# Kernel optimization log

Hardware: AMD Instinct MI355X
Metric: run time of the kernel (lower is better)

Reference implementation:

```python
import jax, jax.numpy as jnp
import numpy as np

# dims: batch B, seq T, model C, expert hidden H, num experts E, top-k K
B, T, C, H, E, K = 4, 1024, 1024, 1024, 8, 2


def _swiglu(x):
    a, b = jnp.split(x, 2, axis=-1)
    return jax.nn.silu(a) * b


def setup_inputs() -> dict:
    key = jax.random.key(0)
    ks = jax.random.split(key, 6)
    s = 0.02
    x = jax.random.normal(ks[0], (B, T, C), jnp.float32)
    # weights stored [in, out] (transpose of torch Linear layout; same math y = x @ W)
    w_shared_in = jax.random.normal(ks[1], (C, 2 * H), jnp.float32) * s
    w_shared_out = jax.random.normal(ks[2], (H, C), jnp.float32) * s
    w1_shared = jax.random.normal(ks[3], (C, 2 * H), jnp.float32) * s
    w2 = jax.random.normal(ks[4], (E, H, C), jnp.float32) * s  # stacked routed_w2
    w_gate = jax.random.normal(ks[5], (C, E), jnp.float32) * s
    gate_bias = jnp.zeros((E,), jnp.float32)  # buffer, updated only in training
    return {
        "x": x,
        "w_shared_in": w_shared_in,
        "w_shared_out": w_shared_out,
        "w1_shared": w1_shared,
        "w2": w2,
        "w_gate": w_gate,
        "gate_bias": gate_bias,
    }


def reference(x, w_shared_in, w_shared_out, w1_shared, w2, w_gate, gate_bias):
    Bx, Tx, Cx = x.shape
    S = Bx * Tx
    fx = x.reshape(S, Cx)  # [S, C]

    # shared expert: SwiGLU MLP
    shared_out = _swiglu(fx @ w_shared_in) @ w_shared_out  # [S, C]

    # router: softmax(top-k) over biased logits
    logits = fx @ w_gate + gate_bias  # [S, E]
    probs = jax.nn.softmax(logits, axis=-1)
    top_val, top_idx = jax.lax.top_k(probs, K)  # [S, K]

    # dense dispatch-weight matrix [S, E] (zero where expert not selected)
    wdense = jnp.zeros((S, E), probs.dtype).at[
        jnp.arange(S)[:, None], top_idx
    ].add(top_val)

    # routed experts share w1_shared, so the SwiGLU hidden is identical for all
    # experts; compute it once for every token, then apply per-expert w2.
    hid = _swiglu(fx @ w1_shared)  # [S, H]
    routed_out = jnp.zeros_like(shared_out)
    for e in range(E):  # small fixed expert count
        routed_out = routed_out + wdense[:, e:e + 1] * (hid @ w2[e])

    return (shared_out + routed_out).reshape(Bx, Tx, Cx)
```

## Files before the change

### kernel.cpp

```cpp
#include <hip/hip_runtime.h>
#include <stdint.h>

typedef __attribute__((ext_vector_type(4))) float f32x4;
typedef __attribute__((ext_vector_type(8))) short s16x8;

static constexpr int S_TOK = 4096;
static constexpr int CDIM  = 1024;
static constexpr int HDIM  = 1024;
static constexpr int H2    = 2048;
static constexpr int NEXP  = 8;

#define MAXRT2 40

__device__ __forceinline__ unsigned short f2bf(float f) {
  union { float f; uint32_t u; } c; c.f = f;
  uint32_t u = c.u;
  u += 0x7fffu + ((u >> 16) & 1u);
  return (unsigned short)(u >> 16);
}

__device__ __forceinline__ float bf2f(unsigned short u) {
  return __uint_as_float(((uint32_t)u) << 16);
}

__device__ __forceinline__ void gload16(const void* g, void* l) {
  __builtin_amdgcn_global_load_lds(
      (const __attribute__((address_space(1))) void*)g,
      (__attribute__((address_space(3))) void*)l, 16, 0, 0);
}

__global__ __launch_bounds__(256) void prep_kernel(
    const float* __restrict__ x, const float* __restrict__ wsi,
    const float* __restrict__ w1s, const float* __restrict__ wso,
    const float* __restrict__ w2,
    unsigned short* __restrict__ xb, unsigned short* __restrict__ w12i,
    unsigned short* __restrict__ wso_t, unsigned short* __restrict__ w2t) {
  __shared__ float t[32][33];
  const int b = blockIdx.x;
  const int tid = threadIdx.x;

  if (b < 512) {
    const int n4 = S_TOK * CDIM / 4;
    for (int i = b * 256 + tid; i < n4; i += 512 * 256) {
      float4 v = reinterpret_cast<const float4*>(x)[i];
      ushort4 o;
      o.x = f2bf(v.x); o.y = f2bf(v.y); o.z = f2bf(v.z); o.w = f2bf(v.w);
      reinterpret_cast<ushort4*>(xb)[i] = o;
    }
    return;
  }
  if (b < 4608) {
    const int b2 = b - 512;
    const float* src = (b2 >= 2048) ? w1s : wsi;
    const int halfoff = (b2 >= 2048) ? 2048 : 0;
    const int rem = b2 & 2047;
    const int r0 = (rem >> 6) * 32;
    const int c0 = (rem & 63) * 32;
#pragma unroll
    for (int i = 0; i < 4; ++i) {
      int idx = tid + i * 256;
      int r = idx >> 5, c = idx & 31;
      t[r][c] = src[(size_t)(r0 + r) * H2 + c0 + c];
    }
    __syncthreads();
#pragma unroll
    for (int i = 0; i < 4; ++i) {
      int idx = tid + i * 256;
      int r = idx >> 5, c = idx & 31;
      const int ccol = c0 + r;
      const int part = ccol >> 10, h = ccol & 1023;
      const int drow = halfoff + (h & 15) + ((h >> 4) << 5) + (part << 4);
      w12i[(size_t)drow * CDIM + r0 + c] = f2bf(t[c][r]);
    }
    return;
  }
  const float* src;
  unsigned short* dst;
  int bx, by;
  if (b < 5632) {
    const int b3 = b - 4608;
    src = wso; dst = wso_t; by = b3 >> 5; bx = b3 & 31;
  } else {
    const int b4 = b - 5632;
    const int z = b4 >> 10;
    const int rem = b4 & 1023;
    src = w2 + (size_t)z * HDIM * CDIM;
    dst = w2t + (size_t)z * HDIM * CDIM;
    by = rem >> 5; bx = rem & 31;
  }
  const int r0 = by * 32, c0 = bx * 32;
#pragma unroll
  for (int i = 0; i < 4; ++i) {
    int idx = tid + i * 256;
    int r = idx >> 5, c = idx & 31;
    t[r][c] = src[(size_t)(r0 + r) * CDIM + c0 + c];
  }
  __syncthreads();
#pragma unroll
  for (int i = 0; i < 4; ++i) {
    int idx = tid + i * 256;
    int r = idx >> 5, c = idx & 31;
    dst[(size_t)(c0 + r) * HDIM + r0 + c] = f2bf(t[c][r]);
  }
}

__global__ void router_kernel(const float* __restrict__ x, const float* __restrict__ wg,
                              const float* __restrict__ gb,
                              int2* __restrict__ ti_e, float2* __restrict__ ti_w) {
  const int l = threadIdx.x & 63;
  const int wid = threadIdx.x >> 6;
  const int s = blockIdx.x * 4 + wid;
  const float* xr = x + (size_t)s * CDIM;
  float acc[NEXP];
#pragma unroll
  for (int e = 0; e < NEXP; ++e) acc[e] = 0.f;
  for (int c = l; c < CDIM; c += 64) {
    float xv = xr[c];
    const float* wr_ = wg + (size_t)c * NEXP;
#pragma unroll
    for (int e = 0; e < NEXP; ++e) acc[e] += xv * wr_[e];
  }
#pragma unroll
  for (int e = 0; e < NEXP; ++e) {
#pragma unroll
    for (int off = 32; off > 0; off >>= 1) acc[e] += __shfl_xor(acc[e], off);
    acc[e] += gb[e];
  }
  float m = acc[0];
#pragma unroll
  for (int e = 1; e < NEXP; ++e) m = fmaxf(m, acc[e]);
  float ex[NEXP], sum = 0.f;
#pragma unroll
  for (int e = 0; e < NEXP; ++e) { ex[e] = __expf(acc[e] - m); sum += ex[e]; }
  int i0 = 0;
#pragma unroll
  for (int e = 1; e < NEXP; ++e) if (acc[e] > acc[i0]) i0 = e;
  int i1 = (i0 == 0) ? 1 : 0;
#pragma unroll
  for (int e = 0; e < NEXP; ++e) {
    if (e == i0) continue;
    if (acc[e] > acc[i1]) i1 = e;
  }
  if (l == 0) {
    const float inv = 1.f / sum;
    ti_e[s] = make_int2(i0, i1);
    ti_w[s] = make_float2(ex[i0] * inv, ex[i1] * inv);
  }
}

__global__ __launch_bounds__(1024) void build_kernel(
    const int2* __restrict__ ti_e,
    int* __restrict__ cnt, int* __restrict__ offs,
    int* __restrict__ gidx, int2* __restrict__ ti_slot) {
  __shared__ int gcnt[64][NEXP];
  __shared__ int gbase[64][NEXP];
  __shared__ int eoff[NEXP];
  const int tid = threadIdx.x;
  const int wid = tid >> 6, lane = tid & 63;

  for (int p = 0; p < 4; ++p) {
    const int g = p * 16 + wid;
    const int2 e = ti_e[g * 64 + lane];
#pragma unroll
    for (int ex = 0; ex < NEXP; ++ex) {
      uint64_t b0 = __ballot(e.x == ex);
      uint64_t b1 = __ballot(e.y == ex);
      if (lane == 0) gcnt[g][ex] = __popcll(b0) + __popcll(b1);
    }
  }
  __syncthreads();
  if (tid < NEXP) {
    const int ex = tid;
    int a = 0;
    for (int g = 0; g < 64; ++g) { gbase[g][ex] = a; a += gcnt[g][ex]; }
    eoff[ex] = a;
  }
  __syncthreads();
  if (tid == 0) {
    int a = 0;
#pragma unroll
    for (int ex = 0; ex < NEXP; ++ex) {
      const int c = eoff[ex];
      offs[ex] = a; cnt[ex] = c; eoff[ex] = a; a += c;
    }
    offs[NEXP] = a;
  }
  __syncthreads();
  for (int p = 0; p < 4; ++p) {
    const int g = p * 16 + wid;
    const int s = g * 64 + lane;
    const int2 e = ti_e[s];
    const uint64_t below = (lane == 0) ? 0ull : (~0ull >> (64 - lane));
    const uint64_t beloweq = below | (1ull << lane);
    int slot0 = 0, slot1 = 0;
#pragma unroll
    for (int ex = 0; ex < NEXP; ++ex) {
      uint64_t b0 = __ballot(e.x == ex);
      uint64_t b1 = __ballot(e.y == ex);
      const int base = gbase[g][ex];
      if (e.x == ex) slot0 = base + __popcll(b0 & below) + __popcll(b1 & below);
      if (e.y == ex) slot1 = base + __popcll(b0 & beloweq) + __popcll(b1 & below);
    }
    ti_slot[s] = make_int2(slot0, slot1);
    gidx[eoff[e.x] + slot0] = s;
    gidx[eoff[e.y] + slot1] = s;
  }
}

template<bool LAST>
__device__ __forceinline__ void iter8(
    const unsigned short* a00, const unsigned short* a01,
    const unsigned short* a10, const unsigned short* a11,
    const unsigned short* b00, const unsigned short* b01,
    const unsigned short* b10, const unsigned short* b11,
    unsigned short* SA, unsigned short* SB,
    int e, int t8, int awb, int bwb, int ak0, int ak1,
    f32x4 (&acc)[8][4]) {
  const int o = e + 1;
  s16x8 a[4][2], bl[2][2], bh[2][2];

#define LD_A4(d, F0) { _Pragma("unroll") for (int f_ = 0; f_ < 4; ++f_) { \
    const unsigned short* p_ = SA + (d) * 16384 + awb + ((F0) + f_) * 1024; \
    a[f_][0] = *reinterpret_cast<const s16x8*>(p_ + ak0); \
    a[f_][1] = *reinterpret_cast<const s16x8*>(p_ + ak1); } }
#define LD_B2(d, bb, N0) { _Pragma("unroll") for (int n_ = 0; n_ < 2; ++n_) { \
    const unsigned short* p_ = SB + (d) * 16384 + bwb + ((N0) + n_) * 1024; \
    bb[n_][0] = *reinterpret_cast<const s16x8*>(p_ + ak0); \
    bb[n_][1] = *reinterpret_cast<const s16x8*>(p_ + ak1); } }
#define STG2(S, d, h, p0, p1, kt) { \
    gload16((p0) + (size_t)(kt) * 64, (S) + (d) * 16384 + (h) * 8192 + t8); \
    gload16((p1) + (size_t)(kt) * 64, (S) + (d) * 16384 + (h) * 8192 + 4096 + t8); }
#define QUAD(F0, bb, N0) { _Pragma("unroll") for (int k_ = 0; k_ < 2; ++k_) \
    { _Pragma("unroll") for (int f_ = 0; f_ < 4; ++f_) \
      { _Pragma("unroll") for (int n_ = 0; n_ < 2; ++n_) \
        acc[(F0) + f_][(N0) + n_] = __builtin_amdgcn_mfma_f32_16x16x32_bf16( \
            a[f_][k_], bb[n_][k_], acc[(F0) + f_][(N0) + n_], 0, 0, 0); } } }
#define PH_MID() { asm volatile("" ::: "memory"); __builtin_amdgcn_s_barrier(); \
    asm volatile("s_waitcnt lgkmcnt(0)" ::: "memory"); __builtin_amdgcn_s_setprio(1); }
#define PH_END() { __builtin_amdgcn_s_setprio(0); asm volatile("" ::: "memory"); \
    __builtin_amdgcn_s_barrier(); asm volatile("" ::: "memory"); }

  LD_A4(0, 0) LD_B2(0, bl, 0)
  STG2(SA, 1, 0, a00, a01, o) STG2(SA, 1, 1, a10, a11, o)
  PH_MID() QUAD(0, bl, 0) PH_END()
  LD_B2(0, bh, 2)
  PH_MID() QUAD(0, bh, 2) PH_END()
  LD_A4(0, 4)
  if (!LAST) STG2(SB, 0, 0, b00, b01, e + 2)
  PH_MID() QUAD(4, bh, 2) PH_END()
  if (!LAST) {
    STG2(SB, 0, 1, b10, b11, e + 2)
    asm volatile("s_waitcnt vmcnt(4)" ::: "memory");
  } else {
    asm volatile("s_waitcnt vmcnt(0)" ::: "memory");
  }
  PH_MID() QUAD(4, bl, 0) PH_END()
  LD_A4(1, 0) LD_B2(1, bl, 0)
  if (!LAST) STG2(SA, 0, 0, a00, a01, e + 2)
  PH_MID() QUAD(0, bl, 0) PH_END()
  LD_B2(1, bh, 2)
  if (!LAST) STG2(SA, 0, 1, a10, a11, e + 2)
  PH_MID() QUAD(0, bh, 2) PH_END()
  LD_A4(1, 4)
  if (!LAST) STG2(SB, 1, 0, b00, b01, o + 2)
  PH_MID() QUAD(4, bh, 2) PH_END()
  if (!LAST) {
    STG2(SB, 1, 1, b10, b11, o + 2)
    asm volatile("s_waitcnt vmcnt(4)" ::: "memory");
  }
  PH_MID() QUAD(4, bl, 0) PH_END()

#undef LD_A4
#undef LD_B2
#undef STG2
#undef QUAD
#undef PH_MID
#undef PH_END
}

__device__ __forceinline__ void prologue8(
    const unsigned short* a00, const unsigned short* a01,
    const unsigned short* a10, const unsigned short* a11,
    const unsigned short* b00, const unsigned short* b01,
    const unsigned short* b10, const unsigned short* b11,
    unsigned short* SA, unsigned short* SB, int t8) {
  gload16(a00, SA + t8);                gload16(a01, SA + 4096 + t8);
  gload16(a10, SA + 8192 + t8);         gload16(a11, SA + 8192 + 4096 + t8);
  gload16(b00, SB + t8);                gload16(b01, SB + 4096 + t8);
  gload16(b10, SB + 8192 + t8);         gload16(b11, SB + 8192 + 4096 + t8);
  gload16(b00 + 64, SB + 16384 + t8);   gload16(b01 + 64, SB + 16384 + 4096 + t8);
  gload16(b10 + 64, SB + 16384 + 8192 + t8);
  gload16(b11 + 64, SB + 16384 + 8192 + 4096 + t8);
  asm volatile("s_waitcnt vmcnt(4)" ::: "memory");
  asm volatile("" ::: "memory");
  __builtin_amdgcn_s_barrier();
  asm volatile("" ::: "memory");
}

__global__ __launch_bounds__(512, 2) void gemm1_kernel(
    const unsigned short* __restrict__ xb, const unsigned short* __restrict__ w12i,
    unsigned short* __restrict__ Hs, unsigned short* __restrict__ Hr) {
  __shared__ unsigned short SA[32768];
  __shared__ unsigned short SB[32768];
  const int tid = threadIdx.x;
  const int l = tid & 63, wid = tid >> 6;
  const int wm = wid >> 2, wn = wid & 3;
  const int lr = l & 15;
  const int awb = wm * 8192 + lr * 64;
  const int bwb = wn * 4096 + lr * 64;
  const int ak0 = (((l >> 4) << 3)) ^ ((l & 7) << 3);
  const int ak1 = 32 ^ ak0;
  const int hw = blockIdx.y * gridDim.x + blockIdx.x;
  const int logical = (hw & 7) * 32 + (hw >> 3);
  const int m0 = (logical >> 4) * 256;
  const int n0 = (logical & 15) * 256;
  const int srow = tid >> 3;
  const int scol = (((tid & 7) ^ (srow & 7)) << 3);
  const int t8 = tid * 8;
  f32x4 acc[8][4] = {};
  const unsigned short* a00 = xb + (size_t)(m0 + srow) * CDIM + scol;
  const unsigned short* a01 = a00 + (size_t)64 * CDIM;
  const unsigned short* a10 = a00 + (size_t)128 * CDIM;
  const unsigned short* a11 = a00 + (size_t)192 * CDIM;
  const unsigned short* b00 = w12i + (size_t)(n0 + srow) * CDIM + scol;
  const unsigned short* b01 = b00 + (size_t)64 * CDIM;
  const unsigned short* b10 = b00 + (size_t)128 * CDIM;
  const unsigned short* b11 = b00 + (size_t)192 * CDIM;

  prologue8(a00, a01, a10, a11, b00, b01, b10, b11, SA, SB, t8);
  for (int it = 0; it < 7; ++it)
    iter8<false>(a00, a01, a10, a11, b00, b01, b10, b11, SA, SB, 2 * it,
                 t8, awb, bwb, ak0, ak1, acc);
  iter8<true>(a00, a01, a10, a11, b00, b01, b10, b11, SA, SB, 14,
              t8, awb, bwb, ak0, ak1, acc);

  unsigned short* Hbuf = (n0 < 2048) ? Hs : Hr;
  const int rb = m0 + wm * 128 + ((l >> 4) << 2);
  const int hbase = ((n0 & 2047) >> 1) + wn * 32;
#pragma unroll
  for (int fm = 0; fm < 8; ++fm)
#pragma unroll
    for (int j = 0; j < 2; ++j)
#pragma unroll
      for (int r = 0; r < 4; ++r) {
        float av = acc[fm][2 * j][r];
        float bv = acc[fm][2 * j + 1][r];
        float hv = (av / (1.f + __expf(-av))) * bv;
        Hbuf[(size_t)(rb + fm * 16 + r) * HDIM + hbase + j * 16 + lr] = f2bf(hv);
      }
}

__global__ __launch_bounds__(512, 2) void gemm2_kernel(
    const unsigned short* __restrict__ Hs, const unsigned short* __restrict__ Hr,
    const unsigned short* __restrict__ wso_t, const unsigned short* __restrict__ w2t,
    const int* __restrict__ cnt, const int* __restrict__ offs, const int* __restrict__ gidx,
    unsigned short* __restrict__ Dout, unsigned short* __restrict__ Eout) {
  __shared__ unsigned short SA[32768];
  __shared__ unsigned short SB[32768];
  const int tid = threadIdx.x;
  const int l = tid & 63, wid = tid >> 6;
  const int wm = wid >> 2, wn = wid & 3;
  const int lr = l & 15;
  const int awb = wm * 8192 + lr * 64;
  const int bwb = wn * 4096 + lr * 64;
  const int ak0 = (((l >> 4) << 3)) ^ ((l & 7) << 3);
  const int ak1 = 32 ^ ak0;
  const int hw = blockIdx.y * gridDim.x + blockIdx.x;
  const int logical = (hw & 7) * 28 + (hw >> 3);
  const int gx = logical >> 2;
  const int n0 = (logical & 3) * 256;
  const int srow = tid >> 3;
  const int scol = (((tid & 7) ^ (srow & 7)) << 3);
  const int t8 = tid * 8;
  f32x4 acc[8][4] = {};

  const unsigned short *a00, *a01, *a10, *a11, *b00, *b01, *b10, *b11;
  int e = 0, cnte = 0, mt = 0, base = 0;
  const bool dense = (gx < 16);
  if (dense) {
    const int m0 = gx * 256;
    a00 = Hs + (size_t)(m0 + srow) * HDIM + scol;
    a01 = a00 + (size_t)64 * HDIM;
    a10 = a00 + (size_t)128 * HDIM;
    a11 = a00 + (size_t)192 * HDIM;
    b00 = wso_t + (size_t)(n0 + srow) * HDIM + scol;
    b01 = b00 + (size_t)64 * HDIM;
    b10 = b00 + (size_t)128 * HDIM;
    b11 = b00 + (size_t)192 * HDIM;
  } else {
    int t = gx - 16;
    bool found = false;
#pragma unroll
    for (int ee = 0; ee < NEXP; ++ee) {
      int c = cnt[ee];
      int nt = (c + 255) >> 8;
      if (!found) {
        if (t < nt) { e = ee; cnte = c; found = true; }
        else t -= nt;
      }
    }
    if (!found) return;
    mt = t;
    base = offs[e];
    const int r0 = mt * 256 + srow;
    const int t0 = gidx[base + min(r0,       cnte - 1)];
    const int t1 = gidx[base + min(r0 + 64,  cnte - 1)];
    const int t2 = gidx[base + min(r0 + 128, cnte - 1)];
    const int t3 = gidx[base + min(r0 + 192, cnte - 1)];
    a00 = Hr + (size_t)t0 * HDIM + scol;
    a01 = Hr + (size_t)t1 * HDIM + scol;
    a10 = Hr + (size_t)t2 * HDIM + scol;
    a11 = Hr + (size_t)t3 * HDIM + scol;
    b00 = w2t + (size_t)e * CDIM * HDIM + (size_t)(n0 + srow) * HDIM + scol;
    b01 = b00 + (size_t)64 * HDIM;
    b10 = b00 + (size_t)128 * HDIM;
    b11 = b00 + (size_t)192 * HDIM;
  }

  prologue8(a00, a01, a10, a11, b00, b01, b10, b11, SA, SB, t8);
  for (int it = 0; it < 7; ++it)
    iter8<false>(a00, a01, a10, a11, b00, b01, b10, b11, SA, SB, 2 * it,
                 t8, awb, bwb, ak0, ak1, acc);
  iter8<true>(a00, a01, a10, a11, b00, b01, b10, b11, SA, SB, 14,
              t8, awb, bwb, ak0, ak1, acc);

  const int rloc0 = wm * 128 + ((l >> 4) << 2);
  const int cb = n0 + wn * 64 + lr;
  if (dense) {
    const int rb = gx * 256 + rloc0;
#pragma unroll
    for (int fm = 0; fm < 8; ++fm)
#pragma unroll
      for (int fn = 0; fn < 4; ++fn)
#pragma unroll
        for (int r = 0; r < 4; ++r)
          Dout[(size_t)(rb + fm * 16 + r) * CDIM + cb + fn * 16] = f2bf(acc[fm][fn][r]);
  } else {
#pragma unroll
    for (int fm = 0; fm < 8; ++fm)
#pragma unroll
      for (int fn = 0; fn < 4; ++fn)
#pragma unroll
        for (int r = 0; r < 4; ++r) {
          const int rloc = mt * 256 + rloc0 + fm * 16 + r;
          if (rloc < cnte)
            Eout[(size_t)(base + rloc) * CDIM + cb + fn * 16] = f2bf(acc[fm][fn][r]);
        }
  }
}

__global__ void scatter_kernel(float* __restrict__ out, const unsigned short* __restrict__ Dout,
                               const unsigned short* __restrict__ Eout,
                               const int2* __restrict__ ti_e, const int2* __restrict__ ti_slot,
                               const float2* __restrict__ ti_w, const int* __restrict__ offs) {
  const int total = S_TOK * (CDIM / 8);
  int i = blockIdx.x * blockDim.x + threadIdx.x;
  const int st = gridDim.x * blockDim.x;
  for (; i < total; i += st) {
    const int s = i >> 7;
    const int j = (i & 127) << 3;
    const int2 e = ti_e[s];
    const int2 sl = ti_slot[s];
    const float2 wv = ti_w[s];
    const int p0 = offs[e.x] + sl.x;
    const int p1 = offs[e.y] + sl.y;
    const ushort4* d0 = reinterpret_cast<const ushort4*>(Dout + (size_t)s * CDIM + j);
    const ushort4* e0 = reinterpret_cast<const ushort4*>(Eout + (size_t)p0 * CDIM + j);
    const ushort4* e1 = reinterpret_cast<const ushort4*>(Eout + (size_t)p1 * CDIM + j);
    float* op = out + (size_t)s * CDIM + j;
#pragma unroll
    for (int q = 0; q < 2; ++q) {
      ushort4 dd = d0[q], a = e0[q], b = e1[q];
      float4 o;
      o.x = bf2f(dd.x) + wv.x * bf2f(a.x) + wv.y * bf2f(b.x);
      o.y = bf2f(dd.y) + wv.x * bf2f(a.y) + wv.y * bf2f(b.y);
      o.z = bf2f(dd.z) + wv.x * bf2f(a.z) + wv.y * bf2f(b.z);
      o.w = bf2f(dd.w) + wv.x * bf2f(a.w) + wv.y * bf2f(b.w);
      reinterpret_cast<float4*>(op)[q] = o;
    }
  }
}

extern "C" void kernel_launch(void* const* d_in, const int* in_sizes, int n_in,
                              void* d_out, int out_size, void* d_ws, size_t ws_size,
                              hipStream_t stream) {
  (void)in_sizes; (void)n_in; (void)out_size; (void)ws_size;
  const float* x   = (const float*)d_in[0];
  const float* wsi = (const float*)d_in[1];
  const float* wso = (const float*)d_in[2];
  const float* w1s = (const float*)d_in[3];
  const float* w2  = (const float*)d_in[4];
  const float* wg  = (const float*)d_in[5];
  const float* gb  = (const float*)d_in[6];
  float* out = (float*)d_out;

  char* w = (char*)d_ws;
  auto alloc = [&](size_t bytes) {
    char* p = w; w += (bytes + 255) & ~(size_t)255; return p;
  };
  unsigned short* xb    = (unsigned short*)alloc((size_t)S_TOK * CDIM * 2);
  unsigned short* w12i  = (unsigned short*)alloc((size_t)2 * H2 * CDIM * 2);
  unsigned short* wso_t = (unsigned short*)alloc((size_t)CDIM * HDIM * 2);
  unsigned short* w2t   = (unsigned short*)alloc((size_t)NEXP * CDIM * HDIM * 2);
  unsigned short* Hs    = (unsigned short*)alloc((size_t)S_TOK * HDIM * 2);
  unsigned short* Hr    = (unsigned short*)alloc((size_t)S_TOK * HDIM * 2);
  unsigned short* Dout  = (unsigned short*)alloc((size_t)S_TOK * CDIM * 2);
  unsigned short* Eout  = (unsigned short*)alloc((size_t)2 * S_TOK * CDIM * 2);
  int2*   ti_e   = (int2*)alloc((size_t)S_TOK * 8);
  int2*   ti_slot= (int2*)alloc((size_t)S_TOK * 8);
  float2* ti_w   = (float2*)alloc((size_t)S_TOK * 8);
  int*    cnt    = (int*)alloc(64);
  int*    offs   = (int*)alloc(64);
  int*    gidx   = (int*)alloc((size_t)2 * S_TOK * 4);

  router_kernel<<<S_TOK / 4, 256, 0, stream>>>(x, wg, gb, ti_e, ti_w);
  build_kernel<<<1, 1024, 0, stream>>>(ti_e, cnt, offs, gidx, ti_slot);

  prep_kernel<<<13824, 256, 0, stream>>>(x, wsi, w1s, wso, w2,
                                         xb, w12i, wso_t, w2t);

  gemm1_kernel<<<dim3(16, 16), 512, 0, stream>>>(xb, w12i, Hs, Hr);

  gemm2_kernel<<<dim3(16 + MAXRT2, CDIM / 256), 512, 0, stream>>>(
      Hs, Hr, wso_t, w2t, cnt, offs, gidx, Dout, Eout);

  scatter_kernel<<<2048, 256, 0, stream>>>(out, Dout, Eout, ti_e, ti_slot, ti_w, offs);
}
```

Baseline: 116.9 us.

## Fuse x bf16 conversion into router; 4-stage K-pipeline in gemm2

The router kernel now writes the bf16 copy of x while it reads x for the gate logits, so prep_kernel no longer makes a second pass over x. gemm2 is rewritten around a 4-slot ring of 32-wide K-chunks in shared memory with three loads in flight, explicit vmcnt waits, and direct global-to-LDS loads spread between MFMA groups under raised wave priority. The launch-bounds occupancy hint is dropped and the LDS swizzle changes. This is meant to hide memory latency better in the main expert GEMM, at the cost of one barrier per 32-K step and more hand-tuned scheduling that is easy to get wrong.

Measured after the change: 114.9 us. About the same (-1.8%).

```diff
diff --git a/kernel.cpp b/kernel.cpp
--- a/kernel.cpp
+++ b/kernel.cpp
@@ -30,30 +30,18 @@
 }
 
 __global__ __launch_bounds__(256) void prep_kernel(
-    const float* __restrict__ x, const float* __restrict__ wsi,
-    const float* __restrict__ w1s, const float* __restrict__ wso,
-    const float* __restrict__ w2,
-    unsigned short* __restrict__ xb, unsigned short* __restrict__ w12i,
-    unsigned short* __restrict__ wso_t, unsigned short* __restrict__ w2t) {
+    const float* __restrict__ wsi, const float* __restrict__ w1s,
+    const float* __restrict__ wso, const float* __restrict__ w2,
+    unsigned short* __restrict__ w12i, unsigned short* __restrict__ wso_t,
+    unsigned short* __restrict__ w2t) {
   __shared__ float t[32][33];
   const int b = blockIdx.x;
   const int tid = threadIdx.x;
 
-  if (b < 512) {
-    const int n4 = S_TOK * CDIM / 4;
-    for (int i = b * 256 + tid; i < n4; i += 512 * 256) {
-      float4 v = reinterpret_cast<const float4*>(x)[i];
-      ushort4 o;
-      o.x = f2bf(v.x); o.y = f2bf(v.y); o.z = f2bf(v.z); o.w = f2bf(v.w);
-      reinterpret_cast<ushort4*>(xb)[i] = o;
-    }
-    return;
-  }
-  if (b < 4608) {
-    const int b2 = b - 512;
-    const float* src = (b2 >= 2048) ? w1s : wsi;
-    const int halfoff = (b2 >= 2048) ? 2048 : 0;
-    const int rem = b2 & 2047;
+  if (b < 4096) {
+    const float* src = (b >= 2048) ? w1s : wsi;
+    const int halfoff = (b >= 2048) ? 2048 : 0;
+    const int rem = b & 2047;
     const int r0 = (rem >> 6) * 32;
     const int c0 = (rem & 63) * 32;
 #pragma unroll
@@ -77,11 +65,11 @@
   const float* src;
   unsigned short* dst;
   int bx, by;
-  if (b < 5632) {
-    const int b3 = b - 4608;
+  if (b < 5120) {
+    const int b3 = b - 4096;
     src = wso; dst = wso_t; by = b3 >> 5; bx = b3 & 31;
   } else {
-    const int b4 = b - 5632;
+    const int b4 = b - 5120;
     const int z = b4 >> 10;
     const int rem = b4 & 1023;
     src = w2 + (size_t)z * HDIM * CDIM;
@@ -106,16 +94,19 @@
 
 __global__ void router_kernel(const float* __restrict__ x, const float* __restrict__ wg,
                               const float* __restrict__ gb,
-                              int2* __restrict__ ti_e, float2* __restrict__ ti_w) {
+                              int2* __restrict__ ti_e, float2* __restrict__ ti_w,
+                              unsigned short* __restrict__ xb) {
   const int l = threadIdx.x & 63;
   const int wid = threadIdx.x >> 6;
   const int s = blockIdx.x * 4 + wid;
   const float* xr = x + (size_t)s * CDIM;
+  unsigned short* xbr = xb + (size_t)s * CDIM;
   float acc[NEXP];
 #pragma unroll
   for (int e = 0; e < NEXP; ++e) acc[e] = 0.f;
   for (int c = l; c < CDIM; c += 64) {
     float xv = xr[c];
+    xbr[c] = f2bf(xv);
     const float* wr_ = wg + (size_t)c * NEXP;
 #pragma unroll
     for (int e = 0; e < NEXP; ++e) acc[e] += xv * wr_[e];
@@ -350,43 +341,38 @@
       }
 }
 
-__global__ __launch_bounds__(512, 2) void gemm2_kernel(
+__global__ __launch_bounds__(512) void gemm2_kernel(
     const unsigned short* __restrict__ Hs, const unsigned short* __restrict__ Hr,
     const unsigned short* __restrict__ wso_t, const unsigned short* __restrict__ w2t,
     const int* __restrict__ cnt, const int* __restrict__ offs, const int* __restrict__ gidx,
     unsigned short* __restrict__ Dout, unsigned short* __restrict__ Eout) {
-  __shared__ unsigned short SA[32768];
-  __shared__ unsigned short SB[32768];
+  __shared__ unsigned short SA[4][2][4096];
+  __shared__ unsigned short SB[4][2][4096];
   const int tid = threadIdx.x;
   const int l = tid & 63, wid = tid >> 6;
   const int wm = wid >> 2, wn = wid & 3;
   const int lr = l & 15;
-  const int awb = wm * 8192 + lr * 64;
-  const int bwb = wn * 4096 + lr * 64;
-  const int ak0 = (((l >> 4) << 3)) ^ ((l & 7) << 3);
-  const int ak1 = 32 ^ ak0;
+  const int hi8 = (l >> 4) << 3;
+  const int wnh = wn >> 1;
+  const int wno = (wn & 1) << 6;
   const int hw = blockIdx.y * gridDim.x + blockIdx.x;
   const int logical = (hw & 7) * 28 + (hw >> 3);
   const int gx = logical >> 2;
   const int n0 = (logical & 3) * 256;
-  const int srow = tid >> 3;
-  const int scol = (((tid & 7) ^ (srow & 7)) << 3);
-  const int t8 = tid * 8;
   f32x4 acc[8][4] = {};
 
-  const unsigned short *a00, *a01, *a10, *a11, *b00, *b01, *b10, *b11;
+  const int srow = tid >> 2;
+  const int cs = (((tid & 3) ^ ((tid >> 3) & 3)) << 3);
+
+  const unsigned short *pa0, *pa1, *pb0, *pb1;
   int e = 0, cnte = 0, mt = 0, base = 0;
   const bool dense = (gx < 16);
   if (dense) {
     const int m0 = gx * 256;
-    a00 = Hs + (size_t)(m0 + srow) * HDIM + scol;
-    a01 = a00 + (size_t)64 * HDIM;
-    a10 = a00 + (size_t)128 * HDIM;
-    a11 = a00 + (size_t)192 * HDIM;
-    b00 = wso_t + (size_t)(n0 + srow) * HDIM + scol;
-    b01 = b00 + (size_t)64 * HDIM;
-    b10 = b00 + (size_t)128 * HDIM;
-    b11 = b00 + (size_t)192 * HDIM;
+    pa0 = Hs + (size_t)(m0 + srow) * HDIM + cs;
+    pa1 = pa0 + (size_t)128 * HDIM;
+    pb0 = wso_t + (size_t)(n0 + srow) * HDIM + cs;
+    pb1 = pb0 + (size_t)128 * HDIM;
   } else {
     int t = gx - 16;
     bool found = false;
@@ -403,26 +389,80 @@
     mt = t;
     base = offs[e];
     const int r0 = mt * 256 + srow;
-    const int t0 = gidx[base + min(r0,       cnte - 1)];
-    const int t1 = gidx[base + min(r0 + 64,  cnte - 1)];
-    const int t2 = gidx[base + min(r0 + 128, cnte - 1)];
-    const int t3 = gidx[base + min(r0 + 192, cnte - 1)];
-    a00 = Hr + (size_t)t0 * HDIM + scol;
-    a01 = Hr + (size_t)t1 * HDIM + scol;
-    a10 = Hr + (size_t)t2 * HDIM + scol;
-    a11 = Hr + (size_t)t3 * HDIM + scol;
-    b00 = w2t + (size_t)e * CDIM * HDIM + (size_t)(n0 + srow) * HDIM + scol;
-    b01 = b00 + (size_t)64 * HDIM;
-    b10 = b00 + (size_t)128 * HDIM;
-    b11 = b00 + (size_t)192 * HDIM;
-  }
-
-  prologue8(a00, a01, a10, a11, b00, b01, b10, b11, SA, SB, t8);
-  for (int it = 0; it < 7; ++it)
-    iter8<false>(a00, a01, a10, a11, b00, b01, b10, b11, SA, SB, 2 * it,
-                 t8, awb, bwb, ak0, ak1, acc);
-  iter8<true>(a00, a01, a10, a11, b00, b01, b10, b11, SA, SB, 14,
-              t8, awb, bwb, ak0, ak1, acc);
+    const int tok0 = gidx[base + min(r0, cnte - 1)];
+    const int tok1 = gidx[base + min(r0 + 128, cnte - 1)];
+    pa0 = Hr + (size_t)tok0 * HDIM + cs;
+    pa1 = Hr + (size_t)tok1 * HDIM + cs;
+    pb0 = w2t + (size_t)e * CDIM * HDIM + (size_t)(n0 + srow) * HDIM + cs;
+    pb1 = pb0 + (size_t)128 * HDIM;
+  }
+
+  const int t8 = tid * 8;
+#pragma unroll
+  for (int s = 0; s < 3; ++s) {
+    const int kk = s * 32;
+    gload16(pa0 + kk, &SA[s][0][t8]);
+    gload16(pa1 + kk, &SA[s][1][t8]);
+    gload16(pb0 + kk, &SB[s][0][t8]);
+    gload16(pb1 + kk, &SB[s][1][t8]);
+  }
+
+  for (int s = 0; s < 32; ++s) {
+    if (s < 30)       asm volatile("s_waitcnt vmcnt(8)" ::: "memory");
+    else if (s == 30) asm volatile("s_waitcnt vmcnt(4)" ::: "memory");
+    else              asm volatile("s_waitcnt vmcnt(0)" ::: "memory");
+    __builtin_amdgcn_s_barrier();
+    asm volatile("" ::: "memory");
+    const int c = s & 3;
+    const unsigned short* A_ = &SA[c][wm][0];
+    const unsigned short* B_ = &SB[c][wnh][0];
+    s16x8 a[8], b[4];
+#pragma unroll
+    for (int f = 0; f < 8; ++f) {
+      const int r = f * 16 + lr;
+      a[f] = *reinterpret_cast<const s16x8*>(&A_[r * 32 + (hi8 ^ (((r >> 1) & 3) << 3))]);
+    }
+#pragma unroll
+    for (int j = 0; j < 4; ++j) {
+      const int r = wno + j * 16 + lr;
+      b[j] = *reinterpret_cast<const s16x8*>(&B_[r * 32 + (hi8 ^ (((r >> 1) & 3) << 3))]);
+    }
+    const int c3 = (s + 3) & 3;
+    const int kk = (s + 3) * 32;
+    const bool st = (s <= 28);
+    if (st) gload16(pa0 + kk, &SA[c3][0][t8]);
+    __builtin_amdgcn_s_setprio(1);
+#pragma unroll
+    for (int f = 0; f < 4; ++f) {
+      acc[f][0] = __builtin_amdgcn_mfma_f32_16x16x32_bf16(a[f], b[0], acc[f][0], 0, 0, 0);
+      acc[f][1] = __builtin_amdgcn_mfma_f32_16x16x32_bf16(a[f], b[1], acc[f][1], 0, 0, 0);
+    }
+    __builtin_amdgcn_s_setprio(0);
+    if (st) gload16(pa1 + kk, &SA[c3][1][t8]);
+    __builtin_amdgcn_s_setprio(1);
+#pragma unroll
+    for (int f = 0; f < 4; ++f) {
+      acc[f][2] = __builtin_amdgcn_mfma_f32_16x16x32_bf16(a[f], b[2], acc[f][2], 0, 0, 0);
+      acc[f][3] = __builtin_amdgcn_mfma_f32_16x16x32_bf16(a[f], b[3], acc[f][3], 0, 0, 0);
+    }
+    __builtin_amdgcn_s_setprio(0);
+    if (st) gload16(pb0 + kk, &SB[c3][0][t8]);
+    __builtin_amdgcn_s_setprio(1);
+#pragma unroll
+    for (int f = 0; f < 4; ++f) {
+      acc[4 + f][0] = __builtin_amdgcn_mfma_f32_16x16x32_bf16(a[4 + f], b[0], acc[4 + f][0], 0, 0, 0);
+      acc[4 + f][1] = __builtin_amdgcn_mfma_f32_16x16x32_bf16(a[4 + f], b[1], acc[4 + f][1], 0, 0, 0);
+    }
+    __builtin_amdgcn_s_setprio(0);
+    if (st) gload16(pb1 + kk, &SB[c3][1][t8]);
+    __builtin_amdgcn_s_setprio(1);
+#pragma unroll
+    for (int f = 0; f < 4; ++f) {
+      acc[4 + f][2] = __builtin_amdgcn_mfma_f32_16x16x32_bf16(a[4 + f], b[2], acc[4 + f][2], 0, 0, 0);
+      acc[4 + f][3] = __builtin_amdgcn_mfma_f32_16x16x32_bf16(a[4 + f], b[3], acc[4 + f][3], 0, 0, 0);
+    }
+    __builtin_amdgcn_s_setprio(0);
+  }
 
   const int rloc0 = wm * 128 + ((l >> 4) << 2);
   const int cb = n0 + wn * 64 + lr;
@@ -513,11 +553,10 @@
   int*    offs   = (int*)alloc(64);
   int*    gidx   = (int*)alloc((size_t)2 * S_TOK * 4);
 
-  router_kernel<<<S_TOK / 4, 256, 0, stream>>>(x, wg, gb, ti_e, ti_w);
+  router_kernel<<<S_TOK / 4, 256, 0, stream>>>(x, wg, gb, ti_e, ti_w, xb);
   build_kernel<<<1, 1024, 0, stream>>>(ti_e, cnt, offs, gidx, ti_slot);
 
-  prep_kernel<<<13824, 256, 0, stream>>>(x, wsi, w1s, wso, w2,
-                                         xb, w12i, wso_t, w2t);
+  prep_kernel<<<13312, 256, 0, stream>>>(wsi, w1s, wso, w2, w12i, wso_t, w2t);
 
   gemm1_kernel<<<dim3(16, 16), 512, 0, stream>>>(xb, w12i, Hs, Hr);
 
```
